# Optimization experiments

Hardware: AMD Instinct MI355X
Metric: run time of the kernel (lower is better)

Reference implementation:

```python
import jax, jax.numpy as jnp
import numpy as np
import math

# B queries, N complex ambient dim, M codebook entries, S payload dim, K quad nodes
B, N, M, S, K = 1024, 128, 8192, 256, 8
EPS_TOTAL = 1e-3
OVERLAP, ANISO = 0.25, 0.75
_t, _w = np.polynomial.hermite.hermgauss(K)
GH_T = jnp.asarray(_t, jnp.float32)
GH_W = jnp.asarray(_w, jnp.float32)


def _init_sigmas():
    # mirrors CPSFFusedCodebook._init_sigmas (log-space for numerical safety at N=128)
    rho = 1.0 + ANISO
    logV = (N / 2.0) * math.log(math.pi) - math.lgamma(N / 2.0 + 1.0)
    log_r = (math.log(OVERLAP) - math.log(M) - logV - math.log(rho)) / N
    r_perp = math.exp(log_r)
    s_perp = 2.0 * math.pi * r_perp ** 2
    return rho * rho * s_perp, s_perp


def setup_inputs() -> dict:
    key = jax.random.key(0)
    ks = jax.random.split(key, 12)
    u = lambda k, sh: jax.random.uniform(k, sh, jnp.float32, -1.0, 1.0)
    s_par, s_perp = _init_sigmas()
    return {
        "z_re": u(ks[0], (B, N)), "z_im": u(ks[1], (B, N)),
        "d_re": u(ks[2], (B, N)), "d_im": u(ks[3], (B, N)),
        "zj_re": 0.5 * u(ks[4], (M, N)), "zj_im": 0.5 * u(ks[5], (M, N)),
        "dj_re": 0.5 * u(ks[6], (M, N)), "dj_im": 0.5 * u(ks[7], (M, N)),
        "T_re": u(ks[8], (M, S)), "T_im": u(ks[9], (M, S)),
        "alpha": jax.random.uniform(ks[10], (M,), jnp.float32, 0.5, 1.5),
        "sigma_par": jnp.full((M,), s_par, jnp.float32),
        "sigma_perp": jnp.full((M,), s_perp, jnp.float32),
    }


def _unit(xr, xi):
    n = jnp.sqrt(jnp.sum(xr * xr + xi * xi, -1, keepdims=True))
    n = jnp.where(n == 0, jnp.ones_like(n), n)
    return xr / n, xi / n


def _forward(z_re, z_im, d_re, d_im, zj_re, zj_im, dj_re, dj_im,
             T_re, T_im, alpha, sigma_par, sigma_perp):
    tiny = jnp.float32(np.finfo(np.float32).tiny)
    dur, dui = _unit(d_re, d_im)          # autonorm_vec_d
    djr, dji = _unit(dj_re, dj_im)        # autonorm_vec_d_j
    a = jnp.maximum(alpha, tiny)
    sp = jnp.maximum(sigma_par, tiny)
    sq = jnp.maximum(sigma_perp, tiny)

    # proj[b,m] = <d_j, z - z_j> (conj-linear in d_j); all via GEMMs, no [B,M,N] tensor
    pr = z_re @ djr.T + z_im @ dji.T - jnp.sum(djr * zj_re + dji * zj_im, -1)[None, :]
    pi = z_im @ djr.T - z_re @ dji.T - jnp.sum(djr * zj_im - dji * zj_re, -1)[None, :]

    # |z - z_j|^2 via GEMM expansion
    dz2 = (jnp.sum(z_re * z_re + z_im * z_im, -1)[:, None]
           + jnp.sum(zj_re * zj_re + zj_im * zj_im, -1)[None, :]
           - 2.0 * (z_re @ zj_re.T + z_im @ zj_im.T))
    perp2 = jnp.maximum(dz2 - (pr * pr + pi * pi), 0.0)  # component orthogonal to d_j

    # Gauss-Hermite quadrature along the codebook direction, scaled per-code
    scale = jnp.sqrt(sp / jnp.pi)                     # [M]
    t = GH_T[None, :] * scale[:, None]                # [M,K] quad offsets
    par2 = (pr[:, :, None] - t[None]) ** 2 + (pi * pi)[:, :, None]   # [B,M,K]
    env = jnp.exp(-jnp.pi * (par2 / sp[None, :, None]
                             + (perp2 / sq[None, :])[:, :, None]))
    rho = jnp.einsum('bmk,k->bm', env, GH_W) * (scale / jnp.sqrt(jnp.pi))[None, :]

    # angular alignment |<d_j, d>|^2
    ar = dur @ djr.T + dui @ dji.T
    ai = dui @ djr.T - dur @ dji.T
    align = ar * ar + ai * ai

    w = a[None, :] * align * rho                      # [B,M] real mixture weights
    den = jnp.sum(w, -1) + EPS_TOTAL                  # [B]
    out_re = (w @ T_re) / den[:, None]                # [B,S]
    out_im = (w @ T_im) / den[:, None]
    return jnp.stack([out_re, out_im], -1)            # [B,S,2] == complex [B,S]


def reference(z_re, z_im, d_re, d_im, zj_re, zj_im, dj_re, dj_im,
              T_re, T_im, alpha, sigma_par, sigma_perp):
    return _forward(z_re, z_im, d_re, d_im, zj_re, zj_im, dj_re, dj_im,
                    T_re, T_im, alpha, sigma_par, sigma_perp)
```

## Files before the change

### kernel.cpp

```cpp
#include <hip/hip_runtime.h>
#include <math.h>

#define Bq 1024
#define Nn 128
#define Mm 8192
#define Ss 256

typedef _Float16 f16;
typedef _Float16 f16x8 __attribute__((ext_vector_type(8)));
typedef _Float16 f16x4 __attribute__((ext_vector_type(4)));
typedef float f32x4 __attribute__((ext_vector_type(4)));

#define PI_F 3.14159265358979323846f
#define INV_SQRT_PI 0.5641895835477563f
#define TINY_F 1.17549435e-38f
#define EPS_TOTAL 1e-3f
#define WSC 1024.0f

#define GLOAD16(g, l) \
    __builtin_amdgcn_global_load_lds((const __attribute__((address_space(1))) void*)(g), \
                                     (__attribute__((address_space(3))) void*)(l), 16, 0, 0)

__global__ void cpsf_prep_pack(
    const float* __restrict__ z_re, const float* __restrict__ z_im,
    const float* __restrict__ d_re, const float* __restrict__ d_im,
    const float* __restrict__ zj_re, const float* __restrict__ zj_im,
    const float* __restrict__ dj_re, const float* __restrict__ dj_im,
    const float* __restrict__ T_re, const float* __restrict__ T_im,
    const float* __restrict__ alpha, const float* __restrict__ sp_,
    const float* __restrict__ sq_, float* __restrict__ z2,
    float* __restrict__ cm, f16* __restrict__ Az, f16* __restrict__ Bp,
    f16* __restrict__ Tt, int Mc, int m0g, int n0, int n1, int n2, int mshift)
{
    __shared__ float tsm[2 * 64 * 65];
    const int bx = blockIdx.x;
    const int tid = threadIdx.x;
    const int wid = tid >> 6;
    const int l = tid & 63;

    if (bx < n0) {
        const int b = bx * 4 + wid;
        const int o = b * Nn;
        float dr0 = d_re[o + l], dr1 = d_re[o + l + 64];
        float di0 = d_im[o + l], di1 = d_im[o + l + 64];
        float zr0 = z_re[o + l], zr1 = z_re[o + l + 64];
        float zi0 = z_im[o + l], zi1 = z_im[o + l + 64];
        float sd = dr0*dr0 + di0*di0 + dr1*dr1 + di1*di1;
        float sz = zr0*zr0 + zi0*zi0 + zr1*zr1 + zi1*zi1;
#pragma unroll
        for (int off = 1; off < 64; off <<= 1) {
            sd += __shfl_xor(sd, off);
            sz += __shfl_xor(sz, off);
        }
        float nd = sqrtf(sd);
        nd = (nd == 0.0f) ? 1.0f : nd;
        float inv = 1.0f / nd;
        if (l == 0) z2[b] = sz;
        int map = l >> 5, c = l & 31;
        int k8 = (c & 15) * 8;
        const float* src = (map == 0) ? ((c < 16) ? z_re : z_im)
                                      : ((c < 16) ? d_re : d_im);
        float s = (map == 0) ? 1.0f : inv;
        float4 v0 = *(const float4*)(src + (size_t)b * Nn + k8);
        float4 v1 = *(const float4*)(src + (size_t)b * Nn + k8 + 4);
        f16x8 ov = {(f16)(v0.x*s), (f16)(v0.y*s), (f16)(v0.z*s), (f16)(v0.w*s),
                    (f16)(v1.x*s), (f16)(v1.y*s), (f16)(v1.z*s), (f16)(v1.w*s)};
        *(f16x8*)(Az + ((size_t)l * 1024 + b) * 8) = ov;
    } else if (bx < n0 + n1) {
        const int m = (bx - n0) * 4 + wid;
        const int o = m * Nn;
        float dr0 = dj_re[o + l], dr1 = dj_re[o + l + 64];
        float di0 = dj_im[o + l], di1 = dj_im[o + l + 64];
        float zr0 = zj_re[o + l], zr1 = zj_re[o + l + 64];
        float zi0 = zj_im[o + l], zi1 = zj_im[o + l + 64];
        float snd = dr0*dr0 + di0*di0 + dr1*dr1 + di1*di1;
        float sc1 = dr0*zr0 + di0*zi0 + dr1*zr1 + di1*zi1;
        float sc2 = dr0*zi0 - di0*zr0 + dr1*zi1 - di1*zr1;
        float sz2 = zr0*zr0 + zi0*zi0 + zr1*zr1 + zi1*zi1;
#pragma unroll
        for (int off = 1; off < 64; off <<= 1) {
            snd += __shfl_xor(snd, off);
            sc1 += __shfl_xor(sc1, off);
            sc2 += __shfl_xor(sc2, off);
            sz2 += __shfl_xor(sz2, off);
        }
        if (l == 0) {
            float nd = sqrtf(snd);
            nd = (nd == 0.0f) ? 1.0f : nd;
            float inv = 1.0f / nd;
            cm[0*Mm + m] = inv;
            cm[1*Mm + m] = sc1 * inv;
            cm[2*Mm + m] = sc2 * inv;
            cm[3*Mm + m] = sz2;
            float sp = fmaxf(sp_[m], TINY_F);
            float sq = fmaxf(sq_[m], TINY_F);
            float sc = sqrtf(sp / PI_F);
            cm[4*Mm + m] = PI_F / sp;
            cm[5*Mm + m] = PI_F / sq;
            cm[6*Mm + m] = fmaxf(alpha[m], TINY_F) * sc * INV_SQRT_PI;
            cm[7*Mm + m] = sc;
        }
    } else if (bx < n0 + n1 + n2) {
        int idx = (bx - n0 - n1) * 256 + tid;
        int m = idx & (Mc - 1);
        int pc = idx >> mshift;
        int p = pc >> 5, c = pc & 31;
        int mg = m0g + m;
        int hi = (c >= 16);
        int k8 = (c & 15) * 8;
        const float* src;
        float sgn = 1.0f;
        if (p == 0)      src = hi ? dj_im : dj_re;
        else if (p == 1) { src = hi ? dj_re : dj_im; sgn = hi ? 1.0f : -1.0f; }
        else             src = hi ? zj_im : zj_re;
        float4 v0 = *(const float4*)(src + (size_t)mg * Nn + k8);
        float4 v1 = *(const float4*)(src + (size_t)mg * Nn + k8 + 4);
        f16x8 o = {(f16)(v0.x*sgn), (f16)(v0.y*sgn), (f16)(v0.z*sgn), (f16)(v0.w*sgn),
                   (f16)(v1.x*sgn), (f16)(v1.y*sgn), (f16)(v1.z*sgn), (f16)(v1.w*sgn)};
        *(f16x8*)(Bp + (size_t)idx * 8) = o;
    } else {
        const int bt = bx - n0 - n1 - n2;
        const int nmb = Mc >> 6;
        const int mb = (bt & (nmb - 1)) * 64, sb = (bt / nmb) * 64;
        float* tr = tsm;
        float* ti = tsm + 64 * 65;
        const int i0 = tid >> 6, jj0 = tid & 63;
#pragma unroll
        for (int it = 0; it < 16; ++it) {
            int i = it * 4 + i0;
            tr[i * 65 + jj0] = T_re[(size_t)(m0g + mb + i) * Ss + sb + jj0];
            ti[i * 65 + jj0] = T_im[(size_t)(m0g + mb + i) * Ss + sb + jj0];
        }
        __syncthreads();
#pragma unroll
        for (int it = 0; it < 16; ++it) {
            int jj = it * 4 + i0;
            int sp = (sb + jj) * 2;
            Tt[(size_t)sp * Mc + mb + jj0]       = (f16)tr[jj0 * 65 + jj];
            Tt[(size_t)(sp + 1) * Mc + mb + jj0] = (f16)ti[jj0 * 65 + jj];
        }
    }
}

__global__ __launch_bounds__(256, 2) void cpsf_gemm_w(
    const f16* __restrict__ Az, const f16* __restrict__ Bp,
    const float* __restrict__ cm, const float* __restrict__ z2v,
    f16* __restrict__ wbuf, float* __restrict__ den, int Mc, int m0g)
{
    __shared__ __align__(16) f16 sm[2 * 1792 * 8];
    const int tid = threadIdx.x;
    const int wid = tid >> 6;
    const int lane = tid & 63;
    const int q = lane >> 4;
    const int li = lane & 15;

    const int nmt = gridDim.x;
    const int sbid = blockIdx.x + nmt * blockIdx.y;
    const int xcd = sbid & 7;
    const int jb = sbid >> 3;
    const int mpg = nmt >> 3;
    const int mtile = xcd * mpg + (jb & (mpg - 1));
    const int btile = jb / mpg;
    const int mb0 = mtile * 64;
    const int bb0 = btile * 128;
    const int wb0 = (wid >> 1) * 64;
    const int wm0 = (wid & 1) * 32;
    const int BUFO = 1792 * 8;

    const f16* gp[7];
    size_t gstep[7];
    f16* lb[7];
#pragma unroll
    for (int i = 0; i < 7; ++i) {
        int c = i * 4 + wid;
        const f16* src;
        size_t st;
        if (c < 8) {
            int g = c >> 1, row = (c & 1) * 64 + lane;
            src = Az + ((size_t)g * 1024 + bb0 + row) * 8;
            st = (size_t)4 * 1024 * 8;
        } else if (c < 16) {
            int c2 = c - 8;
            int g = c2 >> 1, row = (c2 & 1) * 64 + lane;
            src = Az + ((size_t)(32 + g) * 1024 + bb0 + row) * 8;
            st = (size_t)4 * 1024 * 8;
        } else {
            int c2 = c - 16;
            int g = c2 / 3, p = c2 % 3;
            src = Bp + ((size_t)(p * 32 + g) * Mc + mb0 + lane) * 8;
            st = (size_t)4 * Mc * 8;
        }
        gp[i] = src; gstep[i] = st;
        lb[i] = sm + (size_t)(i * 256 + wid * 64) * 8;
    }

    f32x4 accP[4][2][3];
    f32x4 accQ[4][2][2];
#pragma unroll
    for (int t = 0; t < 4; ++t)
#pragma unroll
        for (int u = 0; u < 2; ++u) {
#pragma unroll
            for (int p = 0; p < 3; ++p) accP[t][u][p] = (f32x4){0.f,0.f,0.f,0.f};
#pragma unroll
            for (int p = 0; p < 2; ++p) accQ[t][u][p] = (f32x4){0.f,0.f,0.f,0.f};
        }

#pragma unroll
    for (int i = 0; i < 7; ++i) { GLOAD16(gp[i], lb[i]); gp[i] += gstep[i]; }

#pragma unroll
    for (int ks = 0; ks < 8; ++ks) {
        const int p = ks & 1;
        if (ks > 0) {
            __builtin_amdgcn_sched_barrier(0);
            __builtin_amdgcn_s_barrier();
        }
        if (ks < 7) {
#pragma unroll
            for (int i = 0; i < 7; ++i) { GLOAD16(gp[i], lb[i] + (p ^ 1) * BUFO); gp[i] += gstep[i]; }
            asm volatile("s_waitcnt vmcnt(7)" ::: "memory");
        } else {
            asm volatile("s_waitcnt vmcnt(0)" ::: "memory");
        }
        __builtin_amdgcn_sched_barrier(0);
        __builtin_amdgcn_s_barrier();

        const f16* bs = sm + p * BUFO;
        f16x8 az[4], au[4], bf[3][2];
#pragma unroll
        for (int t = 0; t < 4; ++t) {
            az[t] = *(const f16x8*)(bs + (size_t)(q * 128 + wb0 + t * 16 + li) * 8);
            au[t] = *(const f16x8*)(bs + (size_t)(512 + q * 128 + wb0 + t * 16 + li) * 8);
        }
#pragma unroll
        for (int pp = 0; pp < 3; ++pp)
#pragma unroll
            for (int u = 0; u < 2; ++u)
                bf[pp][u] = *(const f16x8*)(bs + (size_t)(1024 + q * 192 + pp * 64 + wm0 + u * 16 + li) * 8);

        __builtin_amdgcn_s_setprio(1);
#pragma unroll
        for (int t = 0; t < 4; ++t)
#pragma unroll
            for (int u = 0; u < 2; ++u) {
#pragma unroll
                for (int pp = 0; pp < 3; ++pp)
                    accP[t][u][pp] = __builtin_amdgcn_mfma_f32_16x16x32_f16(az[t], bf[pp][u], accP[t][u][pp], 0, 0, 0);
#pragma unroll
                for (int pp = 0; pp < 2; ++pp)
                    accQ[t][u][pp] = __builtin_amdgcn_mfma_f32_16x16x32_f16(au[t], bf[pp][u], accQ[t][u][pp], 0, 0, 0);
            }
        __builtin_amdgcn_s_setprio(0);
    }

    const float GT[8] = {-2.9306374202572440f, -1.9816567566958429f,
                         -1.1571937124467802f, -0.3811869902073221f,
                          0.3811869902073221f,  1.1571937124467802f,
                          1.9816567566958429f,  2.9306374202572440f};
    const float GW[8] = {1.9960407221136762e-04f, 1.7077983007413475e-02f,
                         2.0780232581489188e-01f, 6.6114701255824129e-01f,
                         6.6114701255824129e-01f, 2.0780232581489188e-01f,
                         1.7077983007413475e-02f, 1.9960407221136762e-04f};

    float iv[2], c1[2], c2[2], zj2[2], isp[2], isq[2], cf[2], scl[2];
#pragma unroll
    for (int u = 0; u < 2; ++u) {
        int mg = m0g + mb0 + wm0 + u * 16 + li;
        iv[u]  = cm[0*Mm + mg];
        c1[u]  = cm[1*Mm + mg];  c2[u]  = cm[2*Mm + mg];
        zj2[u] = cm[3*Mm + mg];  isp[u] = cm[4*Mm + mg];
        isq[u] = cm[5*Mm + mg];  cf[u]  = cm[6*Mm + mg];
        scl[u] = cm[7*Mm + mg];
    }

    float dsum[4][4];
#pragma unroll
    for (int t = 0; t < 4; ++t)
#pragma unroll
        for (int r = 0; r < 4; ++r) dsum[t][r] = 0.f;

#pragma unroll
    for (int t = 0; t < 4; ++t) {
#pragma unroll
        for (int r = 0; r < 4; ++r) {
            const int b = bb0 + wb0 + t * 16 + q * 4 + r;
            const float z2b = z2v[b];
#pragma unroll
            for (int u = 0; u < 2; ++u) {
                float pr = accP[t][u][0][r] * iv[u] - c1[u];
                float pi = accP[t][u][1][r] * iv[u] - c2[u];
                float dz2 = z2b + zj2[u] - 2.0f * accP[t][u][2][r];
                float perp2 = fmaxf(dz2 - pr * pr - pi * pi, 0.0f);
                float base = -(isq[u] * perp2 + isp[u] * pi * pi);
                float rho = 0.0f;
#pragma unroll
                for (int k = 0; k < 8; ++k) {
                    float dd = pr - scl[u] * GT[k];
                    rho = fmaf(GW[k], __expf(base - isp[u] * dd * dd), rho);
                }
                float ar = accQ[t][u][0][r] * iv[u], ai = accQ[t][u][1][r] * iv[u];
                float wv = cf[u] * (ar * ar + ai * ai) * rho;
                dsum[t][r] += wv;
                wbuf[(size_t)b * Mc + mb0 + wm0 + u * 16 + li] = (f16)(wv * WSC);
            }
        }
    }
#pragma unroll
    for (int t = 0; t < 4; ++t)
#pragma unroll
        for (int r = 0; r < 4; ++r) {
            float v = dsum[t][r];
            v += __shfl_xor(v, 1);
            v += __shfl_xor(v, 2);
            v += __shfl_xor(v, 4);
            v += __shfl_xor(v, 8);
            if (li == 0) atomicAdd(den + bb0 + wb0 + t * 16 + q * 4 + r, v);
        }
}

__global__ __launch_bounds__(256, 3) void cpsf_gemm_out(
    const f16* __restrict__ wbuf, const f16* __restrict__ Tt,
    float* __restrict__ osl, int Mc, int Kw)
{
    __shared__ __align__(16) f16 sm[2 * 1024 * 8];
    const int tid = threadIdx.x;
    const int wid = tid >> 6;
    const int lane = tid & 63;
    const int q = lane >> 4;
    const int li = lane & 15;
    const int sb0 = blockIdx.x * 128;
    const int bb0 = blockIdx.y * 128;
    const int kz0 = blockIdx.z * Kw;
    float* oz = osl + (size_t)blockIdx.z * ((size_t)Bq * 512);
    const int wb0 = (wid >> 1) * 64;
    const int ws0 = (wid & 1) * 64;
    const int BUFO = 1024 * 8;

    const f16* gp[4];
    f16* lb[4];
#pragma unroll
    for (int i = 0; i < 4; ++i) {
        int c = i * 4 + wid;
        const f16* src;
        if (c < 8) {
            int g = c >> 1, row = (c & 1) * 64 + lane;
            src = wbuf + (size_t)(bb0 + row) * Mc + kz0 + g * 8;
        } else {
            int c2 = c - 8;
            int g = c2 >> 1, row = (c2 & 1) * 64 + lane;
            src = Tt + (size_t)(sb0 + row) * Mc + kz0 + g * 8;
        }
        gp[i] = src;
        lb[i] = sm + (size_t)(i * 256 + wid * 64) * 8;
    }

    f32x4 acc[4][4];
#pragma unroll
    for (int t = 0; t < 4; ++t)
#pragma unroll
        for (int u = 0; u < 4; ++u) acc[t][u] = (f32x4){0.f,0.f,0.f,0.f};

#pragma unroll
    for (int i = 0; i < 4; ++i) { GLOAD16(gp[i], lb[i]); gp[i] += 32; }

    const int nk = Kw >> 5;
    for (int kc = 0; kc < nk; ++kc) {
        const int p = kc & 1;
        if (kc > 0) {
            __builtin_amdgcn_sched_barrier(0);
            __builtin_amdgcn_s_barrier();
        }
        if (kc + 1 < nk) {
#pragma unroll
            for (int i = 0; i < 4; ++i) { GLOAD16(gp[i], lb[i] + (p ^ 1) * BUFO); gp[i] += 32; }
            asm volatile("s_waitcnt vmcnt(4)" ::: "memory");
        } else {
            asm volatile("s_waitcnt vmcnt(0)" ::: "memory");
        }
        __builtin_amdgcn_sched_barrier(0);
        __builtin_amdgcn_s_barrier();

        const f16* bs = sm + p * BUFO;
        f16x8 af[4], bf[4];
#pragma unroll
        for (int t = 0; t < 4; ++t)
            af[t] = *(const f16x8*)(bs + (size_t)(q * 128 + wb0 + t * 16 + li) * 8);
#pragma unroll
        for (int u = 0; u < 4; ++u)
            bf[u] = *(const f16x8*)(bs + (size_t)(512 + q * 128 + ws0 + u * 16 + li) * 8);
        __builtin_amdgcn_s_setprio(1);
#pragma unroll
        for (int t = 0; t < 4; ++t)
#pragma unroll
            for (int u = 0; u < 4; ++u)
                acc[t][u] = __builtin_amdgcn_mfma_f32_16x16x32_f16(af[t], bf[u], acc[t][u], 0, 0, 0);
        __builtin_amdgcn_s_setprio(0);
    }
#pragma unroll
    for (int t = 0; t < 4; ++t)
#pragma unroll
        for (int u = 0; u < 4; ++u)
#pragma unroll
            for (int r = 0; r < 4; ++r)
                oz[(size_t)(bb0 + wb0 + t * 16 + q * 4 + r) * 512 + sb0 + ws0 + u * 16 + li] =
                    acc[t][u][r];
}

__global__ void cpsf_fin(const float* __restrict__ osl, const float* __restrict__ den,
                         float* __restrict__ out, int Z)
{
    int i = blockIdx.x * 256 + threadIdx.x;
    float s = 0.f;
    for (int z = 0; z < Z; ++z) s += osl[(size_t)z * ((size_t)Bq * 512) + i];
    out[i] = s / ((den[i >> 9] + EPS_TOTAL) * WSC);
}

extern "C" void kernel_launch(void* const* d_in, const int* in_sizes, int n_in,
                              void* d_out, int out_size, void* d_ws, size_t ws_size,
                              hipStream_t stream)
{
    (void)in_sizes; (void)n_in; (void)out_size;
    const float* z_re  = (const float*)d_in[0];
    const float* z_im  = (const float*)d_in[1];
    const float* d_re  = (const float*)d_in[2];
    const float* d_im  = (const float*)d_in[3];
    const float* zj_re = (const float*)d_in[4];
    const float* zj_im = (const float*)d_in[5];
    const float* dj_re = (const float*)d_in[6];
    const float* dj_im = (const float*)d_in[7];
    const float* T_re  = (const float*)d_in[8];
    const float* T_im  = (const float*)d_in[9];
    const float* alpha = (const float*)d_in[10];
    const float* s_par = (const float*)d_in[11];
    const float* s_perp= (const float*)d_in[12];

    const size_t SL = (size_t)Bq * 512 * 4;
    const size_t fixedA = 4096 + 4096 + (size_t)8 * Mm * 4 + (size_t)Bq * 512 * 2;

    int Mc = 0, Z = 0;
    const int Zopt[3] = {16, 8, 4};
    const int Mopt[4] = {8192, 4096, 2048, 1024};
    for (int zi = 0; zi < 3 && !Mc; ++zi)
        for (int mi = 0; mi < 4; ++mi) {
            int Zc = Zopt[zi], Mcc = Mopt[mi];
            int nch = Mm / Mcc;
            if (Zc % nch) continue;
            size_t need = (size_t)Zc * SL + fixedA + (size_t)4608 * Mcc;
            if (need <= ws_size) { Mc = Mcc; Z = Zc; break; }
        }
    if (!Mc) { Mc = 1024; Z = 8; }
    const int nch = Mm / Mc;
    const int zs = Z / nch;
    const int Kw = Mc / zs;
    const int mshift = 31 - __builtin_clz((unsigned)Mc);

    char* w8 = (char*)d_ws;
    const size_t o_sl  = 0;
    const size_t o_den = o_sl + (size_t)Z * SL;
    const size_t o_z2  = o_den + 4096;
    const size_t o_cm  = o_z2 + 4096;
    const size_t o_az  = o_cm + (size_t)8 * Mm * 4;
    const size_t o_ch  = o_az + (size_t)Bq * 512 * 2;

    float* osl = (float*)(w8 + o_sl);
    float* den = (float*)(w8 + o_den);
    float* z2  = (float*)(w8 + o_z2);
    float* cm  = (float*)(w8 + o_cm);
    f16*   Az  = (f16*)(w8 + o_az);
    f16*   Bp  = (f16*)(w8 + o_ch);
    f16*   Tt  = (f16*)(w8 + o_ch + (size_t)1536 * Mc);
    f16*   wb  = (f16*)(w8 + o_ch + (size_t)2560 * Mc);

    hipMemsetAsync(w8 + o_den, 0, 4096, stream);

    for (int ci = 0; ci < nch; ++ci) {
        const int m0 = ci * Mc;
        const int n0 = (ci == 0) ? 256 : 0;
        const int n1 = (ci == 0) ? Mm / 4 : 0;
        const int n2 = (96 * Mc) / 256;
        const int n3 = (Mc / 64) * (Ss / 64);
        cpsf_prep_pack<<<n0 + n1 + n2 + n3, 256, 0, stream>>>(
            z_re, z_im, d_re, d_im, zj_re, zj_im, dj_re, dj_im, T_re, T_im,
            alpha, s_par, s_perp, z2, cm, Az, Bp, Tt, Mc, m0, n0, n1, n2, mshift);
        cpsf_gemm_w<<<dim3(Mc / 64, Bq / 128), 256, 0, stream>>>(
            Az, Bp, cm, z2, wb, den, Mc, m0);
        cpsf_gemm_out<<<dim3(4, Bq / 128, zs), 256, 0, stream>>>(
            wb, Tt, osl + (size_t)ci * zs * ((size_t)Bq * 512), Mc, Kw);
    }
    cpsf_fin<<<(Bq * 512) / 256, 256, 0, stream>>>(osl, den, (float*)d_out, Z);
}
```

Measured before the change: 219.8 us.

## Load A operand fragments directly from global into registers, staging only B in LDS

The first GEMM stage no longer stages the query-side A tiles (Az/Au) through shared memory. Each wave loads its own A fragments straight from global memory into a double-buffered register array, while only the codebook-side B tile still uses LDS via global_load_lds. This cuts LDS footprint and LDS traffic for A, which may allow more occupancy. In exchange it raises register pressure and issues more global loads, because A rows are duplicated across waves, and the vmcnt wait counts are hand-tuned to match.

Result: slower. 234.0 us (+6.5%).

```diff
diff --git a/kernel.cpp b/kernel.cpp
--- a/kernel.cpp
+++ b/kernel.cpp
@@ -147,7 +147,7 @@
     const float* __restrict__ cm, const float* __restrict__ z2v,
     f16* __restrict__ wbuf, float* __restrict__ den, int Mc, int m0g)
 {
-    __shared__ __align__(16) f16 sm[2 * 1792 * 8];
+    __shared__ __align__(16) f16 sm[2 * 768 * 8];
     const int tid = threadIdx.x;
     const int wid = tid >> 6;
     const int lane = tid & 63;
@@ -165,34 +165,22 @@
     const int bb0 = btile * 128;
     const int wb0 = (wid >> 1) * 64;
     const int wm0 = (wid & 1) * 32;
-    const int BUFO = 1792 * 8;
-
-    const f16* gp[7];
-    size_t gstep[7];
-    f16* lb[7];
-#pragma unroll
-    for (int i = 0; i < 7; ++i) {
+    const int BUFO = 768 * 8;
+
+    const f16* gp[3];
+    f16* lb[3];
+#pragma unroll
+    for (int i = 0; i < 3; ++i) {
         int c = i * 4 + wid;
-        const f16* src;
-        size_t st;
-        if (c < 8) {
-            int g = c >> 1, row = (c & 1) * 64 + lane;
-            src = Az + ((size_t)g * 1024 + bb0 + row) * 8;
-            st = (size_t)4 * 1024 * 8;
-        } else if (c < 16) {
-            int c2 = c - 8;
-            int g = c2 >> 1, row = (c2 & 1) * 64 + lane;
-            src = Az + ((size_t)(32 + g) * 1024 + bb0 + row) * 8;
-            st = (size_t)4 * 1024 * 8;
-        } else {
-            int c2 = c - 16;
-            int g = c2 / 3, p = c2 % 3;
-            src = Bp + ((size_t)(p * 32 + g) * Mc + mb0 + lane) * 8;
-            st = (size_t)4 * Mc * 8;
-        }
-        gp[i] = src; gstep[i] = st;
-        lb[i] = sm + (size_t)(i * 256 + wid * 64) * 8;
-    }
+        int g = c / 3, p = c % 3;
+        gp[i] = Bp + ((size_t)(p * 32 + g) * Mc + mb0 + lane) * 8;
+        lb[i] = sm + (size_t)(g * 192 + p * 64) * 8;
+    }
+    const size_t KSB = (size_t)4 * Mc * 8;
+
+    const f16* pAz = Az + ((size_t)q * 1024 + bb0 + wb0 + li) * 8;
+    const f16* pAu = pAz + (size_t)32 * 1024 * 8;
+    const size_t KSA = (size_t)4 * 1024 * 8;
 
     f32x4 accP[4][2][3];
     f32x4 accQ[4][2][2];
@@ -206,8 +194,19 @@
             for (int p = 0; p < 2; ++p) accQ[t][u][p] = (f32x4){0.f,0.f,0.f,0.f};
         }
 
-#pragma unroll
-    for (int i = 0; i < 7; ++i) { GLOAD16(gp[i], lb[i]); gp[i] += gstep[i]; }
+    f16x8 azR[2][4], auR[2][4];
+
+#define LOADA(P, KS) do {                                                          \
+    const size_t oA = (size_t)(KS) * KSA;                                          \
+    azR[P][0] = *(const f16x8*)(pAz + oA);       azR[P][1] = *(const f16x8*)(pAz + oA + 128); \
+    azR[P][2] = *(const f16x8*)(pAz + oA + 256); azR[P][3] = *(const f16x8*)(pAz + oA + 384); \
+    auR[P][0] = *(const f16x8*)(pAu + oA);       auR[P][1] = *(const f16x8*)(pAu + oA + 128); \
+    auR[P][2] = *(const f16x8*)(pAu + oA + 256); auR[P][3] = *(const f16x8*)(pAu + oA + 384); \
+} while (0)
+
+#pragma unroll
+    for (int i = 0; i < 3; ++i) { GLOAD16(gp[i], lb[i]); gp[i] += KSB; }
+    LOADA(0, 0);
 
 #pragma unroll
     for (int ks = 0; ks < 8; ++ks) {
@@ -218,8 +217,12 @@
         }
         if (ks < 7) {
 #pragma unroll
-            for (int i = 0; i < 7; ++i) { GLOAD16(gp[i], lb[i] + (p ^ 1) * BUFO); gp[i] += gstep[i]; }
-            asm volatile("s_waitcnt vmcnt(7)" ::: "memory");
+            for (int i = 0; i < 3; ++i) { GLOAD16(gp[i], lb[i] + (p ^ 1) * BUFO); gp[i] += KSB; }
+            if (ks == 0) LOADA(1, 1); else if (ks == 1) LOADA(0, 2);
+            else if (ks == 2) LOADA(1, 3); else if (ks == 3) LOADA(0, 4);
+            else if (ks == 4) LOADA(1, 5); else if (ks == 5) LOADA(0, 6);
+            else LOADA(1, 7);
+            asm volatile("s_waitcnt vmcnt(11)" ::: "memory");
         } else {
             asm volatile("s_waitcnt vmcnt(0)" ::: "memory");
         }
@@ -227,17 +230,12 @@
         __builtin_amdgcn_s_barrier();
 
         const f16* bs = sm + p * BUFO;
-        f16x8 az[4], au[4], bf[3][2];
-#pragma unroll
-        for (int t = 0; t < 4; ++t) {
-            az[t] = *(const f16x8*)(bs + (size_t)(q * 128 + wb0 + t * 16 + li) * 8);
-            au[t] = *(const f16x8*)(bs + (size_t)(512 + q * 128 + wb0 + t * 16 + li) * 8);
-        }
+        f16x8 bf[3][2];
 #pragma unroll
         for (int pp = 0; pp < 3; ++pp)
 #pragma unroll
             for (int u = 0; u < 2; ++u)
-                bf[pp][u] = *(const f16x8*)(bs + (size_t)(1024 + q * 192 + pp * 64 + wm0 + u * 16 + li) * 8);
+                bf[pp][u] = *(const f16x8*)(bs + (size_t)(q * 192 + pp * 64 + wm0 + u * 16 + li) * 8);
 
         __builtin_amdgcn_s_setprio(1);
 #pragma unroll
@@ -246,13 +244,14 @@
             for (int u = 0; u < 2; ++u) {
 #pragma unroll
                 for (int pp = 0; pp < 3; ++pp)
-                    accP[t][u][pp] = __builtin_amdgcn_mfma_f32_16x16x32_f16(az[t], bf[pp][u], accP[t][u][pp], 0, 0, 0);
+                    accP[t][u][pp] = __builtin_amdgcn_mfma_f32_16x16x32_f16(azR[p][t], bf[pp][u], accP[t][u][pp], 0, 0, 0);
 #pragma unroll
                 for (int pp = 0; pp < 2; ++pp)
-                    accQ[t][u][pp] = __builtin_amdgcn_mfma_f32_16x16x32_f16(au[t], bf[pp][u], accQ[t][u][pp], 0, 0, 0);
+                    accQ[t][u][pp] = __builtin_amdgcn_mfma_f32_16x16x32_f16(auR[p][t], bf[pp][u], accQ[t][u][pp], 0, 0, 0);
             }
         __builtin_amdgcn_s_setprio(0);
     }
+#undef LOADA
 
     const float GT[8] = {-2.9306374202572440f, -1.9816567566958429f,
                          -1.1571937124467802f, -0.3811869902073221f,
```

## Double K-tile depth in output GEMM, remap blocks per XCD, vectorize final reduction

Applied to the files above, without the earlier changes.

The output GEMM now stages a 64-wide K slice per iteration (two MFMA sub-steps per barrier pair) with doubled LDS buffers, which halves the number of barriers and raises bytes in flight per load phase. Occupancy is lowered to 2 blocks per CU to make room for the larger LDS. The launch becomes a 1D grid whose block index is remapped so each XCD handles a contiguous set of (batch-tile, K-split) groups, aiming for better L2 reuse of the weight and payload tiles. The final reduction kernel reads and writes float4 and multiplies by a reciprocal, and the config search skips splits that leave fewer than 64 K per block.

Result: faster. 209.1 us (-4.9%).

```diff
diff --git a/kernel.cpp b/kernel.cpp
--- a/kernel.cpp
+++ b/kernel.cpp
@@ -319,40 +319,48 @@
         }
 }
 
-__global__ __launch_bounds__(256, 3) void cpsf_gemm_out(
+__global__ __launch_bounds__(256, 2) void cpsf_gemm_out(
     const f16* __restrict__ wbuf, const f16* __restrict__ Tt,
-    float* __restrict__ osl, int Mc, int Kw)
+    float* __restrict__ osl, int Mc, int Kw, int zs)
 {
-    __shared__ __align__(16) f16 sm[2 * 1024 * 8];
+    __shared__ __align__(16) f16 sm[2 * 2048 * 8];
     const int tid = threadIdx.x;
     const int wid = tid >> 6;
     const int lane = tid & 63;
     const int q = lane >> 4;
     const int li = lane & 15;
-    const int sb0 = blockIdx.x * 128;
-    const int bb0 = blockIdx.y * 128;
-    const int kz0 = blockIdx.z * Kw;
-    float* oz = osl + (size_t)blockIdx.z * ((size_t)Bq * 512);
+
+    const int bid = blockIdx.x;
+    const int xcd = bid & 7;
+    const int j = bid >> 3;
+    const int s = j / zs;
+    const int g = xcd * zs + (j % zs);
+    const int zb = g >> 3;
+    const int yb = g & 7;
+    const int sb0 = s * 128;
+    const int bb0 = yb * 128;
+    const int kz0 = zb * Kw;
+    float* oz = osl + (size_t)zb * ((size_t)Bq * 512);
     const int wb0 = (wid >> 1) * 64;
     const int ws0 = (wid & 1) * 64;
-    const int BUFO = 1024 * 8;
-
-    const f16* gp[4];
-    f16* lb[4];
-#pragma unroll
-    for (int i = 0; i < 4; ++i) {
+    const int BUFO = 2048 * 8;
+
+    const f16* gp[8];
+    f16* lb[8];
+#pragma unroll
+    for (int i = 0; i < 8; ++i) {
         int c = i * 4 + wid;
         const f16* src;
-        if (c < 8) {
-            int g = c >> 1, row = (c & 1) * 64 + lane;
-            src = wbuf + (size_t)(bb0 + row) * Mc + kz0 + g * 8;
+        if (c < 16) {
+            int gch = c >> 1, row = (c & 1) * 64 + lane;
+            src = wbuf + (size_t)(bb0 + row) * Mc + kz0 + gch * 8;
         } else {
-            int c2 = c - 8;
-            int g = c2 >> 1, row = (c2 & 1) * 64 + lane;
-            src = Tt + (size_t)(sb0 + row) * Mc + kz0 + g * 8;
+            int c2 = c - 16;
+            int gch = c2 >> 1, row = (c2 & 1) * 64 + lane;
+            src = Tt + (size_t)(sb0 + row) * Mc + kz0 + gch * 8;
         }
         gp[i] = src;
-        lb[i] = sm + (size_t)(i * 256 + wid * 64) * 8;
+        lb[i] = sm + (size_t)(c * 64) * 8;
     }
 
     f32x4 acc[4][4];
@@ -362,9 +370,9 @@
         for (int u = 0; u < 4; ++u) acc[t][u] = (f32x4){0.f,0.f,0.f,0.f};
 
 #pragma unroll
-    for (int i = 0; i < 4; ++i) { GLOAD16(gp[i], lb[i]); gp[i] += 32; }
-
-    const int nk = Kw >> 5;
+    for (int i = 0; i < 8; ++i) { GLOAD16(gp[i], lb[i]); gp[i] += 64; }
+
+    const int nk = Kw >> 6;
     for (int kc = 0; kc < nk; ++kc) {
         const int p = kc & 1;
         if (kc > 0) {
@@ -373,8 +381,8 @@
         }
         if (kc + 1 < nk) {
 #pragma unroll
-            for (int i = 0; i < 4; ++i) { GLOAD16(gp[i], lb[i] + (p ^ 1) * BUFO); gp[i] += 32; }
-            asm volatile("s_waitcnt vmcnt(4)" ::: "memory");
+            for (int i = 0; i < 8; ++i) { GLOAD16(gp[i], lb[i] + (p ^ 1) * BUFO); gp[i] += 64; }
+            asm volatile("s_waitcnt vmcnt(8)" ::: "memory");
         } else {
             asm volatile("s_waitcnt vmcnt(0)" ::: "memory");
         }
@@ -382,20 +390,23 @@
         __builtin_amdgcn_s_barrier();
 
         const f16* bs = sm + p * BUFO;
-        f16x8 af[4], bf[4];
-#pragma unroll
-        for (int t = 0; t < 4; ++t)
-            af[t] = *(const f16x8*)(bs + (size_t)(q * 128 + wb0 + t * 16 + li) * 8);
-#pragma unroll
-        for (int u = 0; u < 4; ++u)
-            bf[u] = *(const f16x8*)(bs + (size_t)(512 + q * 128 + ws0 + u * 16 + li) * 8);
-        __builtin_amdgcn_s_setprio(1);
-#pragma unroll
-        for (int t = 0; t < 4; ++t)
+#pragma unroll
+        for (int kk = 0; kk < 2; ++kk) {
+            f16x8 af[4], bf[4];
+#pragma unroll
+            for (int t = 0; t < 4; ++t)
+                af[t] = *(const f16x8*)(bs + (size_t)((kk * 4 + q) * 128 + wb0 + t * 16 + li) * 8);
 #pragma unroll
             for (int u = 0; u < 4; ++u)
-                acc[t][u] = __builtin_amdgcn_mfma_f32_16x16x32_f16(af[t], bf[u], acc[t][u], 0, 0, 0);
-        __builtin_amdgcn_s_setprio(0);
+                bf[u] = *(const f16x8*)(bs + (size_t)(1024 + (kk * 4 + q) * 128 + ws0 + u * 16 + li) * 8);
+            __builtin_amdgcn_s_setprio(1);
+#pragma unroll
+            for (int t = 0; t < 4; ++t)
+#pragma unroll
+                for (int u = 0; u < 4; ++u)
+                    acc[t][u] = __builtin_amdgcn_mfma_f32_16x16x32_f16(af[t], bf[u], acc[t][u], 0, 0, 0);
+            __builtin_amdgcn_s_setprio(0);
+        }
     }
 #pragma unroll
     for (int t = 0; t < 4; ++t)
@@ -410,10 +421,15 @@
 __global__ void cpsf_fin(const float* __restrict__ osl, const float* __restrict__ den,
                          float* __restrict__ out, int Z)
 {
-    int i = blockIdx.x * 256 + threadIdx.x;
-    float s = 0.f;
-    for (int z = 0; z < Z; ++z) s += osl[(size_t)z * ((size_t)Bq * 512) + i];
-    out[i] = s / ((den[i >> 9] + EPS_TOTAL) * WSC);
+    int i = (blockIdx.x * 256 + threadIdx.x) * 4;
+    float4 s = {0.f, 0.f, 0.f, 0.f};
+    for (int z = 0; z < Z; ++z) {
+        float4 v = *(const float4*)(osl + (size_t)z * ((size_t)Bq * 512) + i);
+        s.x += v.x; s.y += v.y; s.z += v.z; s.w += v.w;
+    }
+    float d = 1.0f / ((den[i >> 9] + EPS_TOTAL) * WSC);
+    float4 o = {s.x * d, s.y * d, s.z * d, s.w * d};
+    *(float4*)(out + i) = o;
 }
 
 extern "C" void kernel_launch(void* const* d_in, const int* in_sizes, int n_in,
@@ -446,6 +462,7 @@
             int Zc = Zopt[zi], Mcc = Mopt[mi];
             int nch = Mm / Mcc;
             if (Zc % nch) continue;
+            if (Mcc / (Zc / nch) < 64) continue;
             size_t need = (size_t)Zc * SL + fixedA + (size_t)4608 * Mcc;
             if (need <= ws_size) { Mc = Mcc; Z = Zc; break; }
         }
@@ -485,8 +502,8 @@
             alpha, s_par, s_perp, z2, cm, Az, Bp, Tt, Mc, m0, n0, n1, n2, mshift);
         cpsf_gemm_w<<<dim3(Mc / 64, Bq / 128), 256, 0, stream>>>(
             Az, Bp, cm, z2, wb, den, Mc, m0);
-        cpsf_gemm_out<<<dim3(4, Bq / 128, zs), 256, 0, stream>>>(
-            wb, Tt, osl + (size_t)ci * zs * ((size_t)Bq * 512), Mc, Kw);
-    }
-    cpsf_fin<<<(Bq * 512) / 256, 256, 0, stream>>>(osl, den, (float*)d_out, Z);
+        cpsf_gemm_out<<<32 * zs, 256, 0, stream>>>(
+            wb, Tt, osl + (size_t)ci * zs * ((size_t)Bq * 512), Mc, Kw, zs);
+    }
+    cpsf_fin<<<(Bq * 512) / 1024, 256, 0, stream>>>(osl, den, (float*)d_out, Z);
 }
```
